# Performance work log

Hardware: AMD Instinct MI355X
Metric: run time of the kernel (lower is better)

## Reference

```python
import jax, jax.numpy as jnp
import numpy as np

B, A, R, IN, L, P, OUT = 128, 512, 512, 512, 2, 2, 10000


def setup_inputs() -> dict:
    key = jax.random.key(0)
    ks = jax.random.split(key, 24)
    s = 0.02

    def w(k, shape):
        return (jax.random.normal(k, shape, jnp.float32) * s)

    inp = {
        "x": jax.random.normal(ks[0], (B, IN), jnp.float32),
        "att": jax.random.normal(ks[1], (B, A, R), jnp.float32),
        "inputs": jax.random.normal(ks[2], (2 * L, B, R), jnp.float32),
        # first attention
        "a2a_w": w(ks[3], (A, R)), "a2a_b": jnp.zeros((A,), jnp.float32),
        "h2a_w": w(ks[4], (A, R)), "h2a_b": jnp.zeros((A,), jnp.float32),
        "d2d_w": w(ks[5], (1, A)), "d2d_b": jnp.zeros((1,), jnp.float32),
        # second attention
        "a2a1_w": w(ks[6], (A, R)), "a2a1_b": jnp.zeros((A,), jnp.float32),
        "h2a1_w": w(ks[7], (A, R)), "h2a1_b": jnp.zeros((A,), jnp.float32),
        "d2d1_w": w(ks[8], (1, A)), "d2d1_b": jnp.zeros((1,), jnp.float32),
        # stacked LSTM gate weights: [L, P, 4R, feat]
        "i2h_w": w(ks[9], (L, P, 4 * R, IN)), "i2h_b": jnp.zeros((L, P, 4 * R), jnp.float32),
        "h2h_w": w(ks[10], (L, P, 4 * R, R)), "h2h_b": jnp.zeros((L, P, 4 * R), jnp.float32),
        "a2h_w": w(ks[11], (L, P, 4 * R, R)), "a2h_b": jnp.zeros((L, P, 4 * R), jnp.float32),
        # output projection
        "proj_w": w(ks[12], (OUT, R)), "proj_b": jnp.zeros((OUT,), jnp.float32),
    }
    return inp


def _attend(att, h, Wa, ba, Wh, bh, Wd, bd):
    # att: [B, A, R]  h: [B, R]
    v = jnp.einsum('bar,kr->bak', att, Wa) + ba          # [B, A, A]
    hh = h @ Wh.T + bh                                   # [B, A]
    # torch: h.unsqueeze(2).expand_as(v) -> h broadcast along last dim
    dot = jnp.tanh(v + hh[:, :, None])                   # [B, A, A]
    scores = jnp.einsum('bak,k->ba', dot, Wd[0]) + bd[0]  # [B, A]
    weight = jax.nn.softmax(scores, axis=1)              # softmax over dim 1
    att_res = jnp.einsum('bar,ba->br', att, weight)       # [B, R]
    return att_res


def reference(x, att, inputs,
              a2a_w, a2a_b, h2a_w, h2a_b, d2d_w, d2d_b,
              a2a1_w, a2a1_b, h2a1_w, h2a1_b, d2d1_w, d2d1_b,
              i2h_w, i2h_b, h2h_w, h2h_b, a2h_w, a2h_b,
              proj_w, proj_b):
    outputs = []
    for i in range(L):
        prev_c = inputs[2 * i]       # [B, R]
        prev_h = inputs[2 * i + 1]   # [B, R]
        xt = x if i == 0 else x + outputs[-1]
        # attention on previous hidden (dropout is identity: deterministic ref)
        prev_att_res = _attend(att, prev_h, a2a_w, a2a_b, h2a_w, h2a_b, d2d_w, d2d_b)
        # parallel-tower LSTM gates, vectorized over P
        sums = (jnp.einsum('bi,pgi->bpg', xt, i2h_w[i]) + i2h_b[i]
                + jnp.einsum('br,pgr->bpg', prev_h, h2h_w[i]) + h2h_b[i]
                + jnp.einsum('br,pgr->bpg', prev_att_res, a2h_w[i]) + a2h_b[i])  # [B, P, 4R]
        sig = jax.nn.sigmoid(sums[:, :, :3 * R])
        in_gate = sig[:, :, 0:R]
        forget_gate = sig[:, :, R:2 * R]
        out_gate = sig[:, :, 2 * R:3 * R]
        in_transform = jnp.tanh(sums[:, :, 3 * R:4 * R])
        next_c_all = forget_gate * prev_c[:, None, :] + in_gate * in_transform  # [B, P, R]
        next_h_all = out_gate * jnp.tanh(next_c_all)
        next_c = next_c_all.mean(axis=1)  # [B, R]
        next_h = next_h_all.mean(axis=1)
        # second attention on new hidden
        att_res = _attend(att, next_h, a2a1_w, a2a1_b, h2a1_w, h2a1_b, d2d1_w, d2d1_b)
        top_h = att_res + next_h  # dropout disabled (p=0)
        outputs.append(next_c)
        outputs.append(top_h)
    logsoft = jax.nn.log_softmax(outputs[-1] @ proj_w.T + proj_b, axis=1)
    return (jnp.stack(outputs), logsoft)
```

## Files before the change

### kernel.cpp

```cpp
#include <hip/hip_runtime.h>
#include <hip/hip_bf16.h>

#define NB 128
#define NA 512
#define NR 512
#define NOUT 10000

typedef __attribute__((ext_vector_type(8))) short bf16x8;
typedef __attribute__((ext_vector_type(4))) float f32x4;

__device__ inline short f2bf(float f) {
  __hip_bfloat16 h = __float2bfloat16(f);
  return *reinterpret_cast<const short*>(&h);
}

__device__ inline float fast_tanh(float x) {
  float e = __expf(2.0f * x);
  return 1.0f - 2.0f / (e + 1.0f);
}
__device__ inline float fast_sigmoid(float x) {
  return 1.0f / (1.0f + __expf(-x));
}

__device__ inline bf16x8 cvt8(const float* __restrict__ p) {
  f32x4 a = *(const f32x4*)p;
  f32x4 b = *(const f32x4*)(p + 4);
  bf16x8 r;
  r[0] = f2bf(a[0]); r[1] = f2bf(a[1]); r[2] = f2bf(a[2]); r[3] = f2bf(a[3]);
  r[4] = f2bf(b[0]); r[5] = f2bf(b[1]); r[6] = f2bf(b[2]); r[7] = f2bf(b[3]);
  return r;
}

__global__ __launch_bounds__(512) void score_pass(
    const float* __restrict__ att,
    const float* __restrict__ Wa,
    const float* __restrict__ ba,
    const float* __restrict__ Wd,
    const float* __restrict__ hh1,
    const float* __restrict__ hh2,
    float* __restrict__ sc1,
    float* __restrict__ sc2)
{
  __shared__ short Lb[64 * 40];
  __shared__ float sred[8][4][16][2];
  const int tid = threadIdx.x;
  const int wv = tid >> 6;
  const int lane = tid & 63;
  const int l15 = lane & 15, l4 = lane >> 4;
  const int row0 = blockIdx.x * 64;
  const int mrow0 = wv * 64;
  const int scol = tid >> 3, skg = tid & 7;
  const bool has2 = (hh2 != nullptr);

  f32x4 acc[4][4] = {};

  for (int kk = 0; kk < 512; kk += 32) {
    __syncthreads();
    const float4 av = *(const float4*)(att + (size_t)(row0 + scol) * 512 + kk + skg * 4);
    short4 sv;
    sv.x = f2bf(av.x); sv.y = f2bf(av.y); sv.z = f2bf(av.z); sv.w = f2bf(av.w);
    *(short4*)(&Lb[scol * 40 + skg * 4]) = sv;
    __syncthreads();

    bf16x8 afr[4];
#pragma unroll
    for (int mf = 0; mf < 4; mf++)
      afr[mf] = cvt8(Wa + (size_t)(mrow0 + mf * 16 + l15) * 512 + kk + l4 * 8);
    bf16x8 bfr[4];
#pragma unroll
    for (int nf = 0; nf < 4; nf++)
      bfr[nf] = *(const bf16x8*)(&Lb[(nf * 16 + l15) * 40 + l4 * 8]);
#pragma unroll
    for (int mf = 0; mf < 4; mf++)
#pragma unroll
      for (int nf = 0; nf < 4; nf++)
        acc[mf][nf] = __builtin_amdgcn_mfma_f32_16x16x32_bf16(afr[mf], bfr[nf], acc[mf][nf], 0, 0, 0);
  }

  float h1v[4], h2v[4];
#pragma unroll
  for (int nf = 0; nf < 4; nf++) {
    const int colg = row0 + nf * 16 + l15;
    h1v[nf] = hh1[colg];
    h2v[nf] = has2 ? hh2[colg] : 0.f;
  }
  float p1[4] = {0, 0, 0, 0}, p2[4] = {0, 0, 0, 0};
#pragma unroll
  for (int mf = 0; mf < 4; mf++) {
#pragma unroll
    for (int r = 0; r < 4; r++) {
      const int krow = mrow0 + mf * 16 + l4 * 4 + r;
      const float bav = ba[krow];
      const float wdv = Wd[krow];
#pragma unroll
      for (int nf = 0; nf < 4; nf++) {
        const float v = acc[mf][nf][r] + bav;
        p1[nf] += fast_tanh(v + h1v[nf]) * wdv;
        if (has2) p2[nf] += fast_tanh(v + h2v[nf]) * wdv;
      }
    }
  }
#pragma unroll
  for (int nf = 0; nf < 4; nf++) {
    float x1 = p1[nf];
    x1 += __shfl_xor(x1, 16); x1 += __shfl_xor(x1, 32);
    float x2 = p2[nf];
    x2 += __shfl_xor(x2, 16); x2 += __shfl_xor(x2, 32);
    if (l4 == 0) { sred[wv][nf][l15][0] = x1; sred[wv][nf][l15][1] = x2; }
  }
  __syncthreads();
  if (tid < 128) {
    const int v2 = tid >> 6, nf = (tid >> 4) & 3, c = tid & 15;
    if (v2 == 0 || has2) {
      float s = 0.f;
#pragma unroll
      for (int w = 0; w < 8; w++) s += sred[w][nf][c][v2];
      float* dst = v2 ? sc2 : sc1;
      dst[row0 + nf * 16 + c] = s;
    }
  }
}

__global__ __launch_bounds__(256) void gemm_tn512(
    const float* __restrict__ A, const short* __restrict__ Bb,
    const float* __restrict__ bias, float* __restrict__ out,
    const int M, const int Mclamp)
{
  const int tid = threadIdx.x;
  const int wv = tid >> 6, lane = tid & 63;
  const int l15 = lane & 15, l4 = lane >> 4;
  const int mrow0 = blockIdx.x * 256 + wv * 64;
  const int ncol0 = blockIdx.y * 32;
  f32x4 acc[4][2] = {};
  for (int kk = 0; kk < 512; kk += 32) {
    bf16x8 afr[4];
#pragma unroll
    for (int mf = 0; mf < 4; mf++) {
      int row = mrow0 + mf * 16 + l15;
      row = row > Mclamp ? Mclamp : row;
      afr[mf] = cvt8(A + (size_t)row * 512 + kk + l4 * 8);
    }
    bf16x8 bfr[2];
#pragma unroll
    for (int nf = 0; nf < 2; nf++)
      bfr[nf] = *(const bf16x8*)(Bb + (size_t)(ncol0 + nf * 16 + l15) * 512 + kk + l4 * 8);
#pragma unroll
    for (int mf = 0; mf < 4; mf++)
#pragma unroll
      for (int nf = 0; nf < 2; nf++)
        acc[mf][nf] = __builtin_amdgcn_mfma_f32_16x16x32_bf16(afr[mf], bfr[nf], acc[mf][nf], 0, 0, 0);
  }
#pragma unroll
  for (int mf = 0; mf < 4; mf++)
#pragma unroll
    for (int r = 0; r < 4; r++) {
      const int row = mrow0 + mf * 16 + l4 * 4 + r;
      if (row < M) {
        const float bv = bias ? bias[row] : 0.f;
#pragma unroll
        for (int nf = 0; nf < 2; nf++) {
          const int col = ncol0 + nf * 16 + l15;
          out[(size_t)col * M + row] = acc[mf][nf][r] + bv;
        }
      }
    }
}

__global__ __launch_bounds__(256) void gates_gemm(
    const float* __restrict__ A1, const float* __restrict__ A2, const float* __restrict__ A3,
    const short* __restrict__ B1, const short* __restrict__ B2, const short* __restrict__ B3,
    const float* __restrict__ b1, const float* __restrict__ b2, const float* __restrict__ b3,
    float* __restrict__ out)
{
  const int tid = threadIdx.x;
  const int wv = tid >> 6, lane = tid & 63;
  const int l15 = lane & 15, l4 = lane >> 4;
  const int mrow0 = blockIdx.x * 256 + wv * 64;
  const int ncol0 = blockIdx.y * 32;
  f32x4 acc[4][2] = {};
#pragma unroll 1
  for (int seg = 0; seg < 3; seg++) {
    const float* As = seg == 0 ? A1 : (seg == 1 ? A2 : A3);
    const short* Bs = seg == 0 ? B1 : (seg == 1 ? B2 : B3);
    for (int kk = 0; kk < 512; kk += 32) {
      bf16x8 afr[4];
#pragma unroll
      for (int mf = 0; mf < 4; mf++)
        afr[mf] = cvt8(As + (size_t)(mrow0 + mf * 16 + l15) * 512 + kk + l4 * 8);
      bf16x8 bfr[2];
#pragma unroll
      for (int nf = 0; nf < 2; nf++)
        bfr[nf] = *(const bf16x8*)(Bs + (size_t)(ncol0 + nf * 16 + l15) * 512 + kk + l4 * 8);
#pragma unroll
      for (int mf = 0; mf < 4; mf++)
#pragma unroll
        for (int nf = 0; nf < 2; nf++)
          acc[mf][nf] = __builtin_amdgcn_mfma_f32_16x16x32_bf16(afr[mf], bfr[nf], acc[mf][nf], 0, 0, 0);
    }
  }
#pragma unroll
  for (int mf = 0; mf < 4; mf++)
#pragma unroll
    for (int r = 0; r < 4; r++) {
      const int row = mrow0 + mf * 16 + l4 * 4 + r;
      const float bv = b1[row] + b2[row] + b3[row];
#pragma unroll
      for (int nf = 0; nf < 2; nf++) {
        const int col = ncol0 + nf * 16 + l15;
        out[(size_t)col * 4096 + row] = acc[mf][nf][r] + bv;
      }
    }
}

__global__ __launch_bounds__(512) void softmax512(float* __restrict__ d)
{
  const int row = blockIdx.x, t = threadIdx.x;
  const int lane = t & 63, wv = t >> 6;
  __shared__ float red[8];
  float x = d[(size_t)row * 512 + t];
  float m = x;
#pragma unroll
  for (int o = 32; o >= 1; o >>= 1) m = fmaxf(m, __shfl_xor(m, o));
  if (lane == 0) red[wv] = m;
  __syncthreads();
  float gm = red[0];
#pragma unroll
  for (int i = 1; i < 8; i++) gm = fmaxf(gm, red[i]);
  const float e = __expf(x - gm);
  float s = e;
#pragma unroll
  for (int o = 32; o >= 1; o >>= 1) s += __shfl_xor(s, o);
  __syncthreads();
  if (lane == 0) red[wv] = s;
  __syncthreads();
  float gs = 0.f;
#pragma unroll
  for (int i = 0; i < 8; i++) gs += red[i];
  d[(size_t)row * 512 + t] = e / gs;
}

__global__ __launch_bounds__(512) void att_res_pass(
    const float* __restrict__ att,
    const float* __restrict__ w1, const float* __restrict__ w2,
    float* __restrict__ ar1, float* __restrict__ ar2)
{
  const int r = threadIdx.x;
  const int chunk = blockIdx.x;
  const int b = blockIdx.y;
  const bool has2 = (w2 != nullptr);
  float a1 = 0.f, a2 = 0.f;
  const int abase = chunk * 128;
  for (int a = 0; a < 128; a++) {
    const int ai = abase + a;
    const float x = att[((size_t)b * 512 + ai) * 512 + r];
    a1 += x * w1[b * 512 + ai];
    if (has2) a2 += x * w2[b * 512 + ai];
  }
  atomicAdd(&ar1[b * 512 + r], a1);
  if (has2) atomicAdd(&ar2[b * 512 + r], a2);
}

__global__ __launch_bounds__(256) void lstm_combine(
    const float* __restrict__ sums, const float* __restrict__ prev_c,
    float* __restrict__ out_c, float* __restrict__ nh_f, short* __restrict__ nh_bf)
{
  const int idx = blockIdx.x * 256 + threadIdx.x;
  const int b = idx >> 9, r = idx & 511;
  const float* sb = sums + (size_t)b * 4096;
  const float pc = prev_c[idx];
  float nc = 0.f, nh = 0.f;
#pragma unroll
  for (int p = 0; p < 2; p++) {
    const float si = sb[p * 2048 + r];
    const float sf = sb[p * 2048 + 512 + r];
    const float so = sb[p * 2048 + 1024 + r];
    const float st = sb[p * 2048 + 1536 + r];
    const float ig = fast_sigmoid(si), fg = fast_sigmoid(sf), og = fast_sigmoid(so);
    const float it = fast_tanh(st);
    const float c = fg * pc + ig * it;
    const float h = og * fast_tanh(c);
    nc += c; nh += h;
  }
  nc *= 0.5f; nh *= 0.5f;
  out_c[idx] = nc;
  nh_f[idx] = nh;
  nh_bf[idx] = f2bf(nh);
}

__global__ __launch_bounds__(256) void add_store(
    const float* __restrict__ a, const float* __restrict__ b,
    float* __restrict__ of, short* __restrict__ ob)
{
  const int idx = blockIdx.x * 256 + threadIdx.x;
  const float v = a[idx] + b[idx];
  of[idx] = v;
  if (ob) ob[idx] = f2bf(v);
}

__global__ __launch_bounds__(256) void cvt_bf(
    const float* __restrict__ src, const float* __restrict__ add,
    short* __restrict__ dst)
{
  const int idx = blockIdx.x * 256 + threadIdx.x;
  float v = src[idx];
  if (add) v += add[idx];
  dst[idx] = f2bf(v);
}

__global__ __launch_bounds__(256) void logsoftmax_k(
    const float* __restrict__ logits, float* __restrict__ out)
{
  const int b = blockIdx.x, t = threadIdx.x;
  const int lane = t & 63, wv = t >> 6;
  __shared__ float red[4];
  const float* p = logits + (size_t)b * NOUT;
  float m = -3.4e38f;
  for (int j = t; j < NOUT; j += 256) m = fmaxf(m, p[j]);
#pragma unroll
  for (int o = 32; o >= 1; o >>= 1) m = fmaxf(m, __shfl_xor(m, o));
  if (lane == 0) red[wv] = m;
  __syncthreads();
  m = fmaxf(fmaxf(red[0], red[1]), fmaxf(red[2], red[3]));
  float s = 0.f;
  for (int j = t; j < NOUT; j += 256) s += __expf(p[j] - m);
#pragma unroll
  for (int o = 32; o >= 1; o >>= 1) s += __shfl_xor(s, o);
  __syncthreads();
  if (lane == 0) red[wv] = s;
  __syncthreads();
  s = red[0] + red[1] + red[2] + red[3];
  const float lg = m + __logf(s);
  float* q = out + (size_t)b * NOUT;
  for (int j = t; j < NOUT; j += 256) q[j] = p[j] - lg;
}

extern "C" void kernel_launch(void* const* d_in, const int* in_sizes, int n_in,
                              void* d_out, int out_size, void* d_ws, size_t ws_size,
                              hipStream_t stream)
{
  const float* x      = (const float*)d_in[0];
  const float* att    = (const float*)d_in[1];
  const float* inp    = (const float*)d_in[2];
  const float* a2a_w  = (const float*)d_in[3];
  const float* a2a_b  = (const float*)d_in[4];
  const float* h2a_w  = (const float*)d_in[5];
  const float* h2a_b  = (const float*)d_in[6];
  const float* d2d_w  = (const float*)d_in[7];
  const float* a2a1_w = (const float*)d_in[9];
  const float* a2a1_b = (const float*)d_in[10];
  const float* h2a1_w = (const float*)d_in[11];
  const float* h2a1_b = (const float*)d_in[12];
  const float* d2d1_w = (const float*)d_in[13];
  const float* i2h_w  = (const float*)d_in[15];
  const float* i2h_b  = (const float*)d_in[16];
  const float* h2h_w  = (const float*)d_in[17];
  const float* h2h_b  = (const float*)d_in[18];
  const float* a2h_w  = (const float*)d_in[19];
  const float* a2h_b  = (const float*)d_in[20];
  const float* proj_w = (const float*)d_in[21];
  const float* proj_b = (const float*)d_in[22];
  float* out = (float*)d_out;

  const int S = NB * NA;
  float* wsf = (float*)d_ws;
  float* hhA = wsf;
  float* hhB = hhA + S;
  float* hhC = hhB + S;
  float* hhD = hhC + S;
  float* scA = hhD + S;
  float* scB = scA + S;
  float* scC = scB + S;
  float* scD = scC + S;
  float* arA = scD + S;
  float* arB = arA + S;
  float* arC = arB + S;
  float* arD = arC + S;
  float* sums   = arD + S;
  float* logits = sums + NB * 4096;
  float* nh0f   = logits + (size_t)NB * NOUT;
  float* nh1f   = nh0f + S;
  short* bfb    = (short*)(nh1f + S);
  short* xt0b = bfb;
  short* xt1b = xt0b + S;
  short* ph0b = xt1b + S;
  short* ph1b = ph0b + S;
  short* arAb = ph1b + S;
  short* arBb = arAb + S;
  short* nh0b = arBb + S;
  short* nh1b = nh0b + S;
  short* th1b = nh1b + S;

  const float* prev_c0 = inp;
  const float* prev_h0 = inp + S;
  const float* prev_c1 = inp + 2 * S;
  const float* prev_h1 = inp + 3 * S;
  const size_t LSTRIDE_W = (size_t)2 * 2048 * 512;
  const size_t LSTRIDE_B = 4096;

  hipMemsetAsync(arA, 0, (size_t)4 * S * sizeof(float), stream);

  cvt_bf<<<256, 256, 0, stream>>>(x, nullptr, xt0b);
  cvt_bf<<<256, 256, 0, stream>>>(prev_h0, nullptr, ph0b);
  cvt_bf<<<256, 256, 0, stream>>>(prev_h1, nullptr, ph1b);

  gemm_tn512<<<dim3(2, 4), 256, 0, stream>>>(h2a_w, ph0b, h2a_b, hhA, 512, 511);
  gemm_tn512<<<dim3(2, 4), 256, 0, stream>>>(h2a_w, ph1b, h2a_b, hhB, 512, 511);

  score_pass<<<1024, 512, 0, stream>>>(att, a2a_w, a2a_b, d2d_w, hhA, hhB, scA, scB);
  softmax512<<<256, 512, 0, stream>>>(scA);
  att_res_pass<<<dim3(4, 128), 512, 0, stream>>>(att, scA, scB, arA, arB);
  cvt_bf<<<256, 256, 0, stream>>>(arA, nullptr, arAb);
  cvt_bf<<<256, 256, 0, stream>>>(arB, nullptr, arBb);

  gates_gemm<<<dim3(16, 4), 256, 0, stream>>>(
      i2h_w, h2h_w, a2h_w, xt0b, ph0b, arAb, i2h_b, h2h_b, a2h_b, sums);
  lstm_combine<<<256, 256, 0, stream>>>(sums, prev_c0, out , nh0f, nh0b);

  gemm_tn512<<<dim3(2, 4), 256, 0, stream>>>(h2a1_w, nh0b, h2a1_b, hhC, 512, 511);
  score_pass<<<1024, 512, 0, stream>>>(att, a2a1_w, a2a1_b, d2d1_w, hhC, nullptr, scC, nullptr);
  softmax512<<<128, 512, 0, stream>>>(scC);
  att_res_pass<<<dim3(4, 128), 512, 0, stream>>>(att, scC, nullptr, arC, nullptr);
  add_store<<<256, 256, 0, stream>>>(arC, nh0f, out + S , nullptr);
  cvt_bf<<<256, 256, 0, stream>>>(x, out + S, xt1b);

  gates_gemm<<<dim3(16, 4), 256, 0, stream>>>(
      i2h_w + LSTRIDE_W, h2h_w + LSTRIDE_W, a2h_w + LSTRIDE_W,
      xt1b, ph1b, arBb,
      i2h_b + LSTRIDE_B, h2h_b + LSTRIDE_B, a2h_b + LSTRIDE_B, sums);
  lstm_combine<<<256, 256, 0, stream>>>(sums, prev_c1, out + 2 * S , nh1f, nh1b);

  gemm_tn512<<<dim3(2, 4), 256, 0, stream>>>(h2a1_w, nh1b, h2a1_b, hhD, 512, 511);
  score_pass<<<1024, 512, 0, stream>>>(att, a2a1_w, a2a1_b, d2d1_w, hhD, nullptr, scD, nullptr);
  softmax512<<<128, 512, 0, stream>>>(scD);
  att_res_pass<<<dim3(4, 128), 512, 0, stream>>>(att, scD, nullptr, arD, nullptr);
  add_store<<<256, 256, 0, stream>>>(arD, nh1f, out + 3 * S , th1b);

  gemm_tn512<<<dim3(40, 4), 256, 0, stream>>>(proj_w, th1b, proj_b, logits, NOUT, NOUT - 1);
  logsoftmax_k<<<128, 256, 0, stream>>>(logits, out + 4 * S);
}
```

Baseline: 1.048 ms.

## Pre-convert attention tensor and all weights to bf16 once per call

Adds a conversion kernel that writes bf16 copies of att and every weight matrix at the start of each call. The score, gate and projection GEMMs and the weighted-sum pass then read bf16 directly, with no per-tile fp32-to-bf16 conversion. score_pass also drops its LDS staging and block barriers, loads operands straight from global memory, and gets an occupancy hint. The cost is an extra full read of att (128 MB fp32) plus a bf16 write, and att_res_pass now sums bf16-rounded att values, which lowers precision.

New measurement: 1.069 ms. +2.1%, slower.

```diff
diff --git a/kernel.cpp b/kernel.cpp
--- a/kernel.cpp
+++ b/kernel.cpp
@@ -13,7 +13,10 @@
   __hip_bfloat16 h = __float2bfloat16(f);
   return *reinterpret_cast<const short*>(&h);
 }
-
+__device__ inline float bf2f(short s) {
+  unsigned u = (unsigned)(unsigned short)s << 16;
+  return __uint_as_float(u);
+}
 __device__ inline float fast_tanh(float x) {
   float e = __expf(2.0f * x);
   return 1.0f - 2.0f / (e + 1.0f);
@@ -22,18 +25,22 @@
   return 1.0f / (1.0f + __expf(-x));
 }
 
-__device__ inline bf16x8 cvt8(const float* __restrict__ p) {
-  f32x4 a = *(const f32x4*)p;
-  f32x4 b = *(const f32x4*)(p + 4);
+__global__ __launch_bounds__(256) void cvt_f2b(
+    const float* __restrict__ src, short* __restrict__ dst, int n8)
+{
+  const int i = blockIdx.x * 256 + threadIdx.x;
+  if (i >= n8) return;
+  f32x4 a = ((const f32x4*)src)[2 * i];
+  f32x4 b = ((const f32x4*)src)[2 * i + 1];
   bf16x8 r;
   r[0] = f2bf(a[0]); r[1] = f2bf(a[1]); r[2] = f2bf(a[2]); r[3] = f2bf(a[3]);
   r[4] = f2bf(b[0]); r[5] = f2bf(b[1]); r[6] = f2bf(b[2]); r[7] = f2bf(b[3]);
-  return r;
-}
-
-__global__ __launch_bounds__(512) void score_pass(
-    const float* __restrict__ att,
-    const float* __restrict__ Wa,
+  ((bf16x8*)dst)[i] = r;
+}
+
+__global__ __launch_bounds__(512, 4) void score_pass(
+    const short* __restrict__ attb,
+    const short* __restrict__ Wk,
     const float* __restrict__ ba,
     const float* __restrict__ Wd,
     const float* __restrict__ hh1,
@@ -41,7 +48,6 @@
     float* __restrict__ sc1,
     float* __restrict__ sc2)
 {
-  __shared__ short Lb[64 * 40];
   __shared__ float sred[8][4][16][2];
   const int tid = threadIdx.x;
   const int wv = tid >> 6;
@@ -49,27 +55,21 @@
   const int l15 = lane & 15, l4 = lane >> 4;
   const int row0 = blockIdx.x * 64;
   const int mrow0 = wv * 64;
-  const int scol = tid >> 3, skg = tid & 7;
   const bool has2 = (hh2 != nullptr);
 
   f32x4 acc[4][4] = {};
-
+  const short* ap = Wk + (size_t)(mrow0 + l15) * 512 + l4 * 8;
+  const short* bp = attb + (size_t)(row0 + l15) * 512 + l4 * 8;
+
+#pragma unroll 2
   for (int kk = 0; kk < 512; kk += 32) {
-    __syncthreads();
-    const float4 av = *(const float4*)(att + (size_t)(row0 + scol) * 512 + kk + skg * 4);
-    short4 sv;
-    sv.x = f2bf(av.x); sv.y = f2bf(av.y); sv.z = f2bf(av.z); sv.w = f2bf(av.w);
-    *(short4*)(&Lb[scol * 40 + skg * 4]) = sv;
-    __syncthreads();
-
-    bf16x8 afr[4];
+    bf16x8 afr[4], bfr[4];
 #pragma unroll
     for (int mf = 0; mf < 4; mf++)
-      afr[mf] = cvt8(Wa + (size_t)(mrow0 + mf * 16 + l15) * 512 + kk + l4 * 8);
-    bf16x8 bfr[4];
+      afr[mf] = *(const bf16x8*)(ap + mf * 16 * 512 + kk);
 #pragma unroll
     for (int nf = 0; nf < 4; nf++)
-      bfr[nf] = *(const bf16x8*)(&Lb[(nf * 16 + l15) * 40 + l4 * 8]);
+      bfr[nf] = *(const bf16x8*)(bp + (size_t)nf * 16 * 512 + kk);
 #pragma unroll
     for (int mf = 0; mf < 4; mf++)
 #pragma unroll
@@ -122,7 +122,7 @@
 }
 
 __global__ __launch_bounds__(256) void gemm_tn512(
-    const float* __restrict__ A, const short* __restrict__ Bb,
+    const short* __restrict__ Ab, const short* __restrict__ Bb,
     const float* __restrict__ bias, float* __restrict__ out,
     const int M, const int Mclamp)
 {
@@ -138,7 +138,7 @@
     for (int mf = 0; mf < 4; mf++) {
       int row = mrow0 + mf * 16 + l15;
       row = row > Mclamp ? Mclamp : row;
-      afr[mf] = cvt8(A + (size_t)row * 512 + kk + l4 * 8);
+      afr[mf] = *(const bf16x8*)(Ab + (size_t)row * 512 + kk + l4 * 8);
     }
     bf16x8 bfr[2];
 #pragma unroll
@@ -167,7 +167,7 @@
 }
 
 __global__ __launch_bounds__(256) void gates_gemm(
-    const float* __restrict__ A1, const float* __restrict__ A2, const float* __restrict__ A3,
+    const short* __restrict__ A1, const short* __restrict__ A2, const short* __restrict__ A3,
     const short* __restrict__ B1, const short* __restrict__ B2, const short* __restrict__ B3,
     const float* __restrict__ b1, const float* __restrict__ b2, const float* __restrict__ b3,
     float* __restrict__ out)
@@ -180,13 +180,13 @@
   f32x4 acc[4][2] = {};
 #pragma unroll 1
   for (int seg = 0; seg < 3; seg++) {
-    const float* As = seg == 0 ? A1 : (seg == 1 ? A2 : A3);
+    const short* As = seg == 0 ? A1 : (seg == 1 ? A2 : A3);
     const short* Bs = seg == 0 ? B1 : (seg == 1 ? B2 : B3);
     for (int kk = 0; kk < 512; kk += 32) {
       bf16x8 afr[4];
 #pragma unroll
       for (int mf = 0; mf < 4; mf++)
-        afr[mf] = cvt8(As + (size_t)(mrow0 + mf * 16 + l15) * 512 + kk + l4 * 8);
+        afr[mf] = *(const bf16x8*)(As + (size_t)(mrow0 + mf * 16 + l15) * 512 + kk + l4 * 8);
       bf16x8 bfr[2];
 #pragma unroll
       for (int nf = 0; nf < 2; nf++)
@@ -240,7 +240,7 @@
 }
 
 __global__ __launch_bounds__(512) void att_res_pass(
-    const float* __restrict__ att,
+    const short* __restrict__ attb,
     const float* __restrict__ w1, const float* __restrict__ w2,
     float* __restrict__ ar1, float* __restrict__ ar2)
 {
@@ -252,7 +252,7 @@
   const int abase = chunk * 128;
   for (int a = 0; a < 128; a++) {
     const int ai = abase + a;
-    const float x = att[((size_t)b * 512 + ai) * 512 + r];
+    const float x = bf2f(attb[((size_t)b * 512 + ai) * 512 + r]);
     a1 += x * w1[b * 512 + ai];
     if (has2) a2 += x * w2[b * 512 + ai];
   }
@@ -379,8 +379,8 @@
   float* logits = sums + NB * 4096;
   float* nh0f   = logits + (size_t)NB * NOUT;
   float* nh1f   = nh0f + S;
-  short* bfb    = (short*)(nh1f + S);
-  short* xt0b = bfb;
+  short* sreg   = (short*)(nh1f + S);
+  short* xt0b = sreg;
   short* xt1b = xt0b + S;
   short* ph0b = xt1b + S;
   short* ph1b = ph0b + S;
@@ -389,6 +389,15 @@
   short* nh0b = arBb + S;
   short* nh1b = nh0b + S;
   short* th1b = nh1b + S;
+  short* attB  = th1b + S;
+  short* a2aWb = attB + (size_t)S * 512;
+  short* h2aWb = a2aWb + NA * NR;
+  short* a2a1Wb = h2aWb + NA * NR;
+  short* h2a1Wb = a2a1Wb + NA * NR;
+  short* i2hWb = h2a1Wb + NA * NR;
+  short* h2hWb = i2hWb + (size_t)2 * 2 * 2048 * 512;
+  short* a2hWb = h2hWb + (size_t)2 * 2 * 2048 * 512;
+  short* projWb = a2hWb + (size_t)2 * 2 * 2048 * 512;
 
   const float* prev_c0 = inp;
   const float* prev_h0 = inp + S;
@@ -399,42 +408,53 @@
 
   hipMemsetAsync(arA, 0, (size_t)4 * S * sizeof(float), stream);
 
+  cvt_f2b<<<(S * 512 / 8 + 255) / 256, 256, 0, stream>>>(att, attB, S * 512 / 8);
+  cvt_f2b<<<(NA * NR / 8 + 255) / 256, 256, 0, stream>>>(a2a_w, a2aWb, NA * NR / 8);
+  cvt_f2b<<<(NA * NR / 8 + 255) / 256, 256, 0, stream>>>(h2a_w, h2aWb, NA * NR / 8);
+  cvt_f2b<<<(NA * NR / 8 + 255) / 256, 256, 0, stream>>>(a2a1_w, a2a1Wb, NA * NR / 8);
+  cvt_f2b<<<(NA * NR / 8 + 255) / 256, 256, 0, stream>>>(h2a1_w, h2a1Wb, NA * NR / 8);
+  const int WG8 = (int)(2 * LSTRIDE_W / 8);
+  cvt_f2b<<<(WG8 + 255) / 256, 256, 0, stream>>>(i2h_w, i2hWb, WG8);
+  cvt_f2b<<<(WG8 + 255) / 256, 256, 0, stream>>>(h2h_w, h2hWb, WG8);
+  cvt_f2b<<<(WG8 + 255) / 256, 256, 0, stream>>>(a2h_w, a2hWb, WG8);
+  cvt_f2b<<<(NOUT * NR / 8 + 255) / 256, 256, 0, stream>>>(proj_w, projWb, NOUT * NR / 8);
+
   cvt_bf<<<256, 256, 0, stream>>>(x, nullptr, xt0b);
   cvt_bf<<<256, 256, 0, stream>>>(prev_h0, nullptr, ph0b);
   cvt_bf<<<256, 256, 0, stream>>>(prev_h1, nullptr, ph1b);
 
-  gemm_tn512<<<dim3(2, 4), 256, 0, stream>>>(h2a_w, ph0b, h2a_b, hhA, 512, 511);
-  gemm_tn512<<<dim3(2, 4), 256, 0, stream>>>(h2a_w, ph1b, h2a_b, hhB, 512, 511);
-
-  score_pass<<<1024, 512, 0, stream>>>(att, a2a_w, a2a_b, d2d_w, hhA, hhB, scA, scB);
+  gemm_tn512<<<dim3(2, 4), 256, 0, stream>>>(h2aWb, ph0b, h2a_b, hhA, 512, 511);
+  gemm_tn512<<<dim3(2, 4), 256, 0, stream>>>(h2aWb, ph1b, h2a_b, hhB, 512, 511);
+
+  score_pass<<<1024, 512, 0, stream>>>(attB, a2aWb, a2a_b, d2d_w, hhA, hhB, scA, scB);
   softmax512<<<256, 512, 0, stream>>>(scA);
-  att_res_pass<<<dim3(4, 128), 512, 0, stream>>>(att, scA, scB, arA, arB);
+  att_res_pass<<<dim3(4, 128), 512, 0, stream>>>(attB, scA, scB, arA, arB);
   cvt_bf<<<256, 256, 0, stream>>>(arA, nullptr, arAb);
   cvt_bf<<<256, 256, 0, stream>>>(arB, nullptr, arBb);
 
   gates_gemm<<<dim3(16, 4), 256, 0, stream>>>(
-      i2h_w, h2h_w, a2h_w, xt0b, ph0b, arAb, i2h_b, h2h_b, a2h_b, sums);
+      i2hWb, h2hWb, a2hWb, xt0b, ph0b, arAb, i2h_b, h2h_b, a2h_b, sums);
   lstm_combine<<<256, 256, 0, stream>>>(sums, prev_c0, out , nh0f, nh0b);
 
-  gemm_tn512<<<dim3(2, 4), 256, 0, stream>>>(h2a1_w, nh0b, h2a1_b, hhC, 512, 511);
-  score_pass<<<1024, 512, 0, stream>>>(att, a2a1_w, a2a1_b, d2d1_w, hhC, nullptr, scC, nullptr);
+  gemm_tn512<<<dim3(2, 4), 256, 0, stream>>>(h2a1Wb, nh0b, h2a1_b, hhC, 512, 511);
+  score_pass<<<1024, 512, 0, stream>>>(attB, a2a1Wb, a2a1_b, d2d1_w, hhC, nullptr, scC, nullptr);
   softmax512<<<128, 512, 0, stream>>>(scC);
-  att_res_pass<<<dim3(4, 128), 512, 0, stream>>>(att, scC, nullptr, arC, nullptr);
+  att_res_pass<<<dim3(4, 128), 512, 0, stream>>>(attB, scC, nullptr, arC, nullptr);
   add_store<<<256, 256, 0, stream>>>(arC, nh0f, out + S , nullptr);
   cvt_bf<<<256, 256, 0, stream>>>(x, out + S, xt1b);
 
   gates_gemm<<<dim3(16, 4), 256, 0, stream>>>(
-      i2h_w + LSTRIDE_W, h2h_w + LSTRIDE_W, a2h_w + LSTRIDE_W,
+      i2hWb + LSTRIDE_W, h2hWb + LSTRIDE_W, a2hWb + LSTRIDE_W,
       xt1b, ph1b, arBb,
       i2h_b + LSTRIDE_B, h2h_b + LSTRIDE_B, a2h_b + LSTRIDE_B, sums);
   lstm_combine<<<256, 256, 0, stream>>>(sums, prev_c1, out + 2 * S , nh1f, nh1b);
 
-  gemm_tn512<<<dim3(2, 4), 256, 0, stream>>>(h2a1_w, nh1b, h2a1_b, hhD, 512, 511);
-  score_pass<<<1024, 512, 0, stream>>>(att, a2a1_w, a2a1_b, d2d1_w, hhD, nullptr, scD, nullptr);
+  gemm_tn512<<<dim3(2, 4), 256, 0, stream>>>(h2a1Wb, nh1b, h2a1_b, hhD, 512, 511);
+  score_pass<<<1024, 512, 0, stream>>>(attB, a2a1Wb, a2a1_b, d2d1_w, hhD, nullptr, scD, nullptr);
   softmax512<<<128, 512, 0, stream>>>(scD);
-  att_res_pass<<<dim3(4, 128), 512, 0, stream>>>(att, scD, nullptr, arD, nullptr);
+  att_res_pass<<<dim3(4, 128), 512, 0, stream>>>(attB, scD, nullptr, arD, nullptr);
   add_store<<<256, 256, 0, stream>>>(arD, nh1f, out + 3 * S , th1b);
 
-  gemm_tn512<<<dim3(40, 4), 256, 0, stream>>>(proj_w, th1b, proj_b, logits, NOUT, NOUT - 1);
+  gemm_tn512<<<dim3(40, 4), 256, 0, stream>>>(projWb, th1b, proj_b, logits, NOUT, NOUT - 1);
   logsoftmax_k<<<128, 256, 0, stream>>>(logits, out + 4 * S);
 }
```
